# Kernel tuning notes

Hardware: AMD Instinct MI355X
Metric: run time of the kernel (lower is better)

## Reference

```python
import jax, jax.numpy as jnp
import numpy as np
from jax import lax

B, T, V, E, H, O = 32, 64, 30000, 64, 64, 7


def setup_inputs() -> dict:
    key = jax.random.key(0)
    ks = jax.random.split(key, 17)
    s_in = 1.0 / np.sqrt(E)
    s_h = 1.0 / np.sqrt(H)
    inp = {
        "x": jax.random.uniform(ks[0], (B, T, V), dtype=jnp.float32),
        "vocab_embed": 0.02 * jax.random.normal(ks[1], (V, E), dtype=jnp.float32),
        "W_ir": s_in * jax.random.normal(ks[2], (H, E), dtype=jnp.float32),
        "W_iz": s_in * jax.random.normal(ks[3], (H, E), dtype=jnp.float32),
        "W_in": s_in * jax.random.normal(ks[4], (H, E), dtype=jnp.float32),
        "W_hr": s_h * jax.random.normal(ks[5], (H, H), dtype=jnp.float32),
        "W_hz": s_h * jax.random.normal(ks[6], (H, H), dtype=jnp.float32),
        "W_hn": s_h * jax.random.normal(ks[7], (H, H), dtype=jnp.float32),
        "b_ir": s_h * jax.random.normal(ks[8], (H,), dtype=jnp.float32),
        "b_iz": s_h * jax.random.normal(ks[9], (H,), dtype=jnp.float32),
        "b_in": s_h * jax.random.normal(ks[10], (H,), dtype=jnp.float32),
        "b_hr": s_h * jax.random.normal(ks[11], (H,), dtype=jnp.float32),
        "b_hz": s_h * jax.random.normal(ks[12], (H,), dtype=jnp.float32),
        "b_hn": s_h * jax.random.normal(ks[13], (H,), dtype=jnp.float32),
        "W_out": s_h * jax.random.normal(ks[14], (O, H), dtype=jnp.float32),
        "b_out": s_h * jax.random.normal(ks[15], (O,), dtype=jnp.float32),
        "prediction_point": T,
    }
    return inp


def reference(x, vocab_embed, W_ir, W_iz, W_in, W_hr, W_hz, W_hn,
              b_ir, b_iz, b_in, b_hr, b_hz, b_hn, W_out, b_out,
              prediction_point):
    # embed_x = relu((x @ vocab_embed) / x.sum(-1, keepdims))  -> [B, T, E]
    embed_x = jax.nn.relu(jnp.einsum("btv,ve->bte", x, vocab_embed)
                          / jnp.sum(x, axis=2, keepdims=True))

    # t = 0: no hidden contribution at all (faithful to original)
    e0 = embed_x[:, 0, :]
    z1 = jax.nn.sigmoid(e0 @ W_iz.T + b_iz)
    n1 = jnp.tanh(e0 @ W_in.T + b_in)
    h0 = (1.0 - z1) * n1  # [B, H]

    def step(h, e_t):
        hr = h @ W_hr.T + b_hr
        r = jax.nn.sigmoid(e_t @ W_ir.T + b_ir + hr)
        z = jax.nn.sigmoid(e_t @ W_iz.T + b_iz + h @ W_hz.T + b_hz)
        # NOTE: original code uses hidden_reset (W_hr) here, not hidden_new
        n = jnp.tanh(e_t @ W_in.T + b_in + r * hr)
        h_new = (1.0 - z) * n + z * h
        return h_new, None

    # scan over t = 1 .. prediction_point-1
    es = jnp.swapaxes(embed_x[:, 1:prediction_point, :], 0, 1)  # [T-1, B, E]
    h_final, _ = lax.scan(step, h0, es)

    return h_final @ W_out.T + b_out  # [B, O] logits (prob=False)
```

## Files before the change

### kernel.cpp

```cpp
#include <hip/hip_runtime.h>
#include <hip/hip_bf16.h>

typedef unsigned short u16;
typedef short short8 __attribute__((ext_vector_type(8)));
typedef float floatx4 __attribute__((ext_vector_type(4)));

#define BB 32
#define TT 64
#define VV 30000
#define EE 64
#define HH 64
#define OO 7
#define KSPLIT 32
#define NU32 937
#define KTAIL0 29984

__device__ __forceinline__ u16 f2b(float f) {
    unsigned u = __float_as_uint(f);
    u += 0x7FFFu + ((u >> 16) & 1u);
    return (u16)(u >> 16);
}

__device__ __forceinline__ float sigmoid_f(float x) {
    return 1.f / (1.f + __expf(-x));
}

__device__ __forceinline__ float tanh_f(float x) {
    float a = fabsf(x);
    float e = __expf(-2.f * a);
    float t = (1.f - e) / (1.f + e);
    return x < 0.f ? -t : t;
}

__global__ __launch_bounds__(256) void kT(const float* __restrict__ VE, u16* __restrict__ VT) {
    __shared__ u16 tile[64][72];
    int v0 = blockIdx.x * 64;
    int t = threadIdx.x;
    #pragma unroll
    for (int i = 0; i < 4; ++i) {
        int c = i * 256 + t;
        int row = c >> 4, col4 = (c & 15) * 4;
        if (v0 + row < VV) {
            float4 d = *(const float4*)(VE + (size_t)(v0 + row) * EE + col4);
            ushort4 s;
            s.x = f2b(d.x); s.y = f2b(d.y); s.z = f2b(d.z); s.w = f2b(d.w);
            *(ushort4*)&tile[row][col4] = s;
        }
    }
    __syncthreads();
    int e0 = (t >> 6) * 16;
    int v = t & 63;
    if (v0 + v < VV) {
        #pragma unroll
        for (int ee = 0; ee < 16; ++ee) {
            int e = e0 + ee;
            VT[(size_t)e * VV + v0 + v] = tile[v][e];
        }
    }
}

__global__ __launch_bounds__(256) void kE(const float* __restrict__ x, const u16* __restrict__ vt,
                                          float* __restrict__ Cpart, float* __restrict__ Rpart) {
    int tid = threadIdx.x;
    int w = tid >> 6, l = tid & 63;
    int r15 = l & 15, q = l >> 4;
    int mb = blockIdx.x, kb = blockIdx.y;
    int m0 = mb * 64;
    int wr = m0 + w * 16;

    const float* aRow = x + (size_t)(wr + r15) * VV;
    const u16* b0p = vt + (size_t)(r15)      * VV;
    const u16* b1p = vt + (size_t)(16 + r15) * VV;
    const u16* b2p = vt + (size_t)(32 + r15) * VV;
    const u16* b3p = vt + (size_t)(48 + r15) * VV;

    floatx4 acc[4] = {};
    floatx4 accS = {};
    short8 ones;
    #pragma unroll
    for (int i = 0; i < 8; ++i) ones[i] = (short)0x3F80;

    int u0 = (kb * NU32) / KSPLIT, u1 = ((kb + 1) * NU32) / KSPLIT;

    #pragma unroll 2
    for (int u = u0; u < u1; ++u) {
        int k0 = u * 32 + q * 8;
        float4 a0 = *(const float4*)(aRow + k0);
        float4 a1 = *(const float4*)(aRow + k0 + 4);
        short8 bf0 = *(const short8*)(b0p + k0);
        short8 bf1 = *(const short8*)(b1p + k0);
        short8 bf2 = *(const short8*)(b2p + k0);
        short8 bf3 = *(const short8*)(b3p + k0);
        short8 af;
        af[0] = (short)f2b(a0.x); af[1] = (short)f2b(a0.y);
        af[2] = (short)f2b(a0.z); af[3] = (short)f2b(a0.w);
        af[4] = (short)f2b(a1.x); af[5] = (short)f2b(a1.y);
        af[6] = (short)f2b(a1.z); af[7] = (short)f2b(a1.w);
        acc[0] = __builtin_amdgcn_mfma_f32_16x16x32_bf16(af, bf0, acc[0], 0, 0, 0);
        acc[1] = __builtin_amdgcn_mfma_f32_16x16x32_bf16(af, bf1, acc[1], 0, 0, 0);
        acc[2] = __builtin_amdgcn_mfma_f32_16x16x32_bf16(af, bf2, acc[2], 0, 0, 0);
        acc[3] = __builtin_amdgcn_mfma_f32_16x16x32_bf16(af, bf3, acc[3], 0, 0, 0);
        accS   = __builtin_amdgcn_mfma_f32_16x16x32_bf16(af, ones, accS, 0, 0, 0);
    }

    if (kb == KSPLIT - 1) {
        short8 af, bf0, bf1, bf2, bf3;
        #pragma unroll
        for (int i = 0; i < 8; ++i) { af[i] = 0; bf0[i] = 0; bf1[i] = 0; bf2[i] = 0; bf3[i] = 0; }
        if (q < 2) {
            int k0 = KTAIL0 + q * 8;
            float4 a0 = *(const float4*)(aRow + k0);
            float4 a1 = *(const float4*)(aRow + k0 + 4);
            af[0] = (short)f2b(a0.x); af[1] = (short)f2b(a0.y);
            af[2] = (short)f2b(a0.z); af[3] = (short)f2b(a0.w);
            af[4] = (short)f2b(a1.x); af[5] = (short)f2b(a1.y);
            af[6] = (short)f2b(a1.z); af[7] = (short)f2b(a1.w);
            bf0 = *(const short8*)(b0p + k0);
            bf1 = *(const short8*)(b1p + k0);
            bf2 = *(const short8*)(b2p + k0);
            bf3 = *(const short8*)(b3p + k0);
        }
        acc[0] = __builtin_amdgcn_mfma_f32_16x16x32_bf16(af, bf0, acc[0], 0, 0, 0);
        acc[1] = __builtin_amdgcn_mfma_f32_16x16x32_bf16(af, bf1, acc[1], 0, 0, 0);
        acc[2] = __builtin_amdgcn_mfma_f32_16x16x32_bf16(af, bf2, acc[2], 0, 0, 0);
        acc[3] = __builtin_amdgcn_mfma_f32_16x16x32_bf16(af, bf3, acc[3], 0, 0, 0);
        accS   = __builtin_amdgcn_mfma_f32_16x16x32_bf16(af, ones, accS, 0, 0, 0);
    }

    float* Cp = Cpart + (size_t)kb * (2048 * 64);
    #pragma unroll
    for (int r = 0; r < 4; ++r) {
        int row = wr + q * 4 + r;
        #pragma unroll
        for (int n = 0; n < 4; ++n)
            Cp[(size_t)row * 64 + n * 16 + r15] = acc[n][r];
        if (r15 == 0) Rpart[kb * 2048 + row] = accS[r];
    }
}

__global__ __launch_bounds__(64) void kG(const float* __restrict__ Cpart, const float* __restrict__ Rpart,
                                         const float* __restrict__ Wir, const float* __restrict__ Wiz,
                                         const float* __restrict__ Win,
                                         const float* __restrict__ bir, const float* __restrict__ biz,
                                         const float* __restrict__ bin,
                                         float* __restrict__ Xr, float* __restrict__ Xz,
                                         float* __restrict__ Xn, float* __restrict__ H0) {
    int m = blockIdx.x;
    int j = threadIdx.x;
    __shared__ float e[64];
    float c = 0.f, rs = 0.f;
    #pragma unroll
    for (int kb = 0; kb < KSPLIT; ++kb) {
        c  += Cpart[(size_t)kb * 2048 * 64 + m * 64 + j];
        rs += Rpart[kb * 2048 + m];
    }
    float ev = c / rs;
    e[j] = ev > 0.f ? ev : 0.f;
    __syncthreads();
    float ar = bir[j], az = biz[j], an = bin[j];
    #pragma unroll 4
    for (int i = 0; i < 64; ++i) {
        float ei = e[i];
        ar += ei * Wir[j * 64 + i];
        az += ei * Wiz[j * 64 + i];
        an += ei * Win[j * 64 + i];
    }
    Xr[m * 64 + j] = ar;
    Xz[m * 64 + j] = az;
    Xn[m * 64 + j] = an;
    if ((m & 63) == 0) {
        int b = m >> 6;
        float z1 = sigmoid_f(az);
        float n1 = tanh_f(an);
        H0[b * 64 + j] = (1.f - z1) * n1;
    }
}

__global__ __launch_bounds__(256) void kS(const float* __restrict__ Xr, const float* __restrict__ Xz,
                                          const float* __restrict__ Xn, const float* __restrict__ H0,
                                          const float* __restrict__ Whr, const float* __restrict__ Whz,
                                          const float* __restrict__ bhr, const float* __restrict__ bhz,
                                          const float* __restrict__ Wout, const float* __restrict__ bout,
                                          float* __restrict__ out) {
    int b = blockIdx.x;
    int tid = threadIdx.x;
    int i = tid & 63, jw = tid >> 6;
    __shared__ float XsR[64 * 64], XsZ[64 * 64], XsN[64 * 64];
    __shared__ float h[64];
    __shared__ float P[4][2][64];

    const float* xr = Xr + (size_t)b * 4096;
    const float* xz = Xz + (size_t)b * 4096;
    const float* xn = Xn + (size_t)b * 4096;
    #pragma unroll
    for (int it = 0; it < 4; ++it) {
        int off = it * 1024 + tid * 4;
        *(float4*)&XsR[off] = *(const float4*)&xr[off];
        *(float4*)&XsZ[off] = *(const float4*)&xz[off];
        *(float4*)&XsN[off] = *(const float4*)&xn[off];
    }
    float wr[16], wz[16];
    #pragma unroll
    for (int jj = 0; jj < 16; ++jj) {
        wr[jj] = Whr[i * 64 + jw * 16 + jj];
        wz[jj] = Whz[i * 64 + jw * 16 + jj];
    }
    float bhr_i = bhr[i];
    float bhz_i = bhz[i];
    if (tid < 64) h[tid] = H0[b * 64 + tid];
    __syncthreads();

    for (int t = 1; t < 64; ++t) {
        float pr = 0.f, pz = 0.f;
        #pragma unroll
        for (int jj = 0; jj < 16; ++jj) {
            float hj = h[jw * 16 + jj];
            pr += hj * wr[jj];
            pz += hj * wz[jj];
        }
        P[jw][0][i] = pr;
        P[jw][1][i] = pz;
        __syncthreads();
        if (tid < 64) {
            float hr = bhr_i + P[0][0][i] + P[1][0][i] + P[2][0][i] + P[3][0][i];
            float hz = bhz_i + P[0][1][i] + P[1][1][i] + P[2][1][i] + P[3][1][i];
            float r = sigmoid_f(XsR[t * 64 + i] + hr);
            float z = sigmoid_f(XsZ[t * 64 + i] + hz);
            float n = tanh_f(XsN[t * 64 + i] + r * hr);
            h[i] = (1.f - z) * n + z * h[i];
        }
        __syncthreads();
    }

    if (tid < OO) {
        float acc2 = bout[tid];
        #pragma unroll 8
        for (int ii = 0; ii < 64; ++ii)
            acc2 += h[ii] * Wout[tid * 64 + ii];
        out[b * OO + tid] = acc2;
    }
}

extern "C" void kernel_launch(void* const* d_in, const int* in_sizes, int n_in,
                              void* d_out, int out_size, void* d_ws, size_t ws_size,
                              hipStream_t stream) {
    const float* x    = (const float*)d_in[0];
    const float* VE   = (const float*)d_in[1];
    const float* Wir  = (const float*)d_in[2];
    const float* Wiz  = (const float*)d_in[3];
    const float* Win  = (const float*)d_in[4];
    const float* Whr  = (const float*)d_in[5];
    const float* Whz  = (const float*)d_in[6];
    const float* bir  = (const float*)d_in[8];
    const float* biz  = (const float*)d_in[9];
    const float* bin  = (const float*)d_in[10];
    const float* bhr  = (const float*)d_in[11];
    const float* bhz  = (const float*)d_in[12];
    const float* Wout = (const float*)d_in[14];
    const float* bout = (const float*)d_in[15];

    char* ws = (char*)d_ws;
    u16*   VT    = (u16*)(ws);
    float* Cpart = (float*)(ws + 3840000);
    float* Rpart = (float*)(ws + 3840000 + 16777216);
    float* Xr    = (float*)(ws + 20879360);
    float* Xz    = (float*)(ws + 21403648);
    float* Xn    = (float*)(ws + 21927936);
    float* H0    = (float*)(ws + 22452224);

    kT<<<(VV + 63) / 64, 256, 0, stream>>>(VE, VT);
    kE<<<dim3(2048 / 64, KSPLIT), 256, 0, stream>>>(x, VT, Cpart, Rpart);
    kG<<<2048, 64, 0, stream>>>(Cpart, Rpart, Wir, Wiz, Win, bir, biz, bin, Xr, Xz, Xn, H0);
    kS<<<BB, 256, 0, stream>>>(Xr, Xz, Xn, H0, Whr, Whz, bhr, bhz, Wout, bout, (float*)d_out);
}
```

Before: 450.2 us.

## Pack bf16 with byte-permute truncation and rewrite gate projection with MFMA

In the main embedding GEMM, the per-element round-to-nearest fp32→bf16 conversion is replaced by a single byte-permute that packs the high halves of two floats. This cuts VALU work in the inner loop but switches to truncation, which adds a small rounding bias. The input-gate projection kernel is rewritten to handle 64 rows per block. It reduces the split-K partials with float4 loads, stages normalized, ReLU'd embeddings in LDS as bf16, and computes all three gate projections with MFMA instead of scalar FMA loops. This lowers instruction count and launch granularity, but it runs only 32 blocks to stream the 16 MB partial buffer and uses bf16 weights in place of fp32.

```diff
diff --git a/kernel.cpp b/kernel.cpp
--- a/kernel.cpp
+++ b/kernel.cpp
@@ -19,6 +19,10 @@
     unsigned u = __float_as_uint(f);
     u += 0x7FFFu + ((u >> 16) & 1u);
     return (u16)(u >> 16);
+}
+
+__device__ __forceinline__ unsigned pk2(float fo, float fe) {
+    return __builtin_amdgcn_perm(__float_as_uint(fo), __float_as_uint(fe), 0x07060302u);
 }
 
 __device__ __forceinline__ float sigmoid_f(float x) {
@@ -92,10 +96,11 @@
         short8 bf2 = *(const short8*)(b2p + k0);
         short8 bf3 = *(const short8*)(b3p + k0);
         short8 af;
-        af[0] = (short)f2b(a0.x); af[1] = (short)f2b(a0.y);
-        af[2] = (short)f2b(a0.z); af[3] = (short)f2b(a0.w);
-        af[4] = (short)f2b(a1.x); af[5] = (short)f2b(a1.y);
-        af[6] = (short)f2b(a1.z); af[7] = (short)f2b(a1.w);
+        unsigned* afu = (unsigned*)&af;
+        afu[0] = pk2(a0.y, a0.x);
+        afu[1] = pk2(a0.w, a0.z);
+        afu[2] = pk2(a1.y, a1.x);
+        afu[3] = pk2(a1.w, a1.z);
         acc[0] = __builtin_amdgcn_mfma_f32_16x16x32_bf16(af, bf0, acc[0], 0, 0, 0);
         acc[1] = __builtin_amdgcn_mfma_f32_16x16x32_bf16(af, bf1, acc[1], 0, 0, 0);
         acc[2] = __builtin_amdgcn_mfma_f32_16x16x32_bf16(af, bf2, acc[2], 0, 0, 0);
@@ -111,10 +116,11 @@
             int k0 = KTAIL0 + q * 8;
             float4 a0 = *(const float4*)(aRow + k0);
             float4 a1 = *(const float4*)(aRow + k0 + 4);
-            af[0] = (short)f2b(a0.x); af[1] = (short)f2b(a0.y);
-            af[2] = (short)f2b(a0.z); af[3] = (short)f2b(a0.w);
-            af[4] = (short)f2b(a1.x); af[5] = (short)f2b(a1.y);
-            af[6] = (short)f2b(a1.z); af[7] = (short)f2b(a1.w);
+            unsigned* afu = (unsigned*)&af;
+            afu[0] = pk2(a0.y, a0.x);
+            afu[1] = pk2(a0.w, a0.z);
+            afu[2] = pk2(a1.y, a1.x);
+            afu[3] = pk2(a1.w, a1.z);
             bf0 = *(const short8*)(b0p + k0);
             bf1 = *(const short8*)(b1p + k0);
             bf2 = *(const short8*)(b2p + k0);
@@ -138,41 +144,102 @@
     }
 }
 
-__global__ __launch_bounds__(64) void kG(const float* __restrict__ Cpart, const float* __restrict__ Rpart,
-                                         const float* __restrict__ Wir, const float* __restrict__ Wiz,
-                                         const float* __restrict__ Win,
-                                         const float* __restrict__ bir, const float* __restrict__ biz,
-                                         const float* __restrict__ bin,
-                                         float* __restrict__ Xr, float* __restrict__ Xz,
-                                         float* __restrict__ Xn, float* __restrict__ H0) {
-    int m = blockIdx.x;
-    int j = threadIdx.x;
-    __shared__ float e[64];
-    float c = 0.f, rs = 0.f;
-    #pragma unroll
+__global__ __launch_bounds__(256) void kG2(const float* __restrict__ Cpart, const float* __restrict__ Rpart,
+                                           const float* __restrict__ Wir, const float* __restrict__ Wiz,
+                                           const float* __restrict__ Win,
+                                           const float* __restrict__ bir, const float* __restrict__ biz,
+                                           const float* __restrict__ bin,
+                                           float* __restrict__ Xr, float* __restrict__ Xz,
+                                           float* __restrict__ Xn, float* __restrict__ H0) {
+    __shared__ __align__(16) u16 eL[64 * 72];
+    __shared__ float rsinv[64];
+    int tid = threadIdx.x;
+    int m0 = blockIdx.x * 64;
+
+    if (tid < 64) {
+        float rs = 0.f;
+        #pragma unroll
+        for (int kb = 0; kb < KSPLIT; ++kb)
+            rs += Rpart[kb * 2048 + m0 + tid];
+        rsinv[tid] = 1.f / rs;
+    }
+    float4 a4[4];
+    #pragma unroll
+    for (int r = 0; r < 4; ++r) { a4[r].x = 0.f; a4[r].y = 0.f; a4[r].z = 0.f; a4[r].w = 0.f; }
+    const float* cp = Cpart + (size_t)m0 * 64 + tid * 4;
+    #pragma unroll 4
     for (int kb = 0; kb < KSPLIT; ++kb) {
-        c  += Cpart[(size_t)kb * 2048 * 64 + m * 64 + j];
-        rs += Rpart[kb * 2048 + m];
-    }
-    float ev = c / rs;
-    e[j] = ev > 0.f ? ev : 0.f;
+        #pragma unroll
+        for (int r = 0; r < 4; ++r) {
+            float4 v = *(const float4*)(cp + (size_t)kb * (2048 * 64) + r * 1024);
+            a4[r].x += v.x; a4[r].y += v.y; a4[r].z += v.z; a4[r].w += v.w;
+        }
+    }
     __syncthreads();
-    float ar = bir[j], az = biz[j], an = bin[j];
-    #pragma unroll 4
-    for (int i = 0; i < 64; ++i) {
-        float ei = e[i];
-        ar += ei * Wir[j * 64 + i];
-        az += ei * Wiz[j * 64 + i];
-        an += ei * Win[j * 64 + i];
-    }
-    Xr[m * 64 + j] = ar;
-    Xz[m * 64 + j] = az;
-    Xn[m * 64 + j] = an;
-    if ((m & 63) == 0) {
-        int b = m >> 6;
-        float z1 = sigmoid_f(az);
-        float n1 = tanh_f(an);
-        H0[b * 64 + j] = (1.f - z1) * n1;
+    #pragma unroll
+    for (int r = 0; r < 4; ++r) {
+        int m = r * 16 + (tid >> 4);
+        float ri = rsinv[m];
+        float e0 = a4[r].x * ri, e1 = a4[r].y * ri, e2 = a4[r].z * ri, e3 = a4[r].w * ri;
+        e0 = e0 > 0.f ? e0 : 0.f;  e1 = e1 > 0.f ? e1 : 0.f;
+        e2 = e2 > 0.f ? e2 : 0.f;  e3 = e3 > 0.f ? e3 : 0.f;
+        ushort4 s;
+        s.x = f2b(e0); s.y = f2b(e1); s.z = f2b(e2); s.w = f2b(e3);
+        *(ushort4*)&eL[m * 72 + (tid & 15) * 4] = s;
+    }
+    __syncthreads();
+
+    int w = tid >> 6, l = tid & 63;
+    int r15 = l & 15, q = l >> 4;
+    short8 a0 = *(const short8*)&eL[(w * 16 + r15) * 72 + q * 8];
+    short8 a1 = *(const short8*)&eL[(w * 16 + r15) * 72 + 32 + q * 8];
+
+    floatx4 acc[3][4] = {};
+    const float* Wg0 = Wir; const float* Wg1 = Wiz; const float* Wg2 = Win;
+    #pragma unroll
+    for (int g = 0; g < 3; ++g) {
+        const float* W = (g == 0) ? Wg0 : (g == 1) ? Wg1 : Wg2;
+        #pragma unroll
+        for (int nb = 0; nb < 4; ++nb) {
+            const float* wrow = W + (nb * 16 + r15) * 64 + q * 8;
+            float4 w0 = *(const float4*)(wrow);
+            float4 w1 = *(const float4*)(wrow + 4);
+            float4 w2 = *(const float4*)(wrow + 32);
+            float4 w3 = *(const float4*)(wrow + 36);
+            short8 b0, b1;
+            unsigned* b0u = (unsigned*)&b0; unsigned* b1u = (unsigned*)&b1;
+            b0u[0] = pk2(w0.y, w0.x); b0u[1] = pk2(w0.w, w0.z);
+            b0u[2] = pk2(w1.y, w1.x); b0u[3] = pk2(w1.w, w1.z);
+            b1u[0] = pk2(w2.y, w2.x); b1u[1] = pk2(w2.w, w2.z);
+            b1u[2] = pk2(w3.y, w3.x); b1u[3] = pk2(w3.w, w3.z);
+            acc[g][nb] = __builtin_amdgcn_mfma_f32_16x16x32_bf16(a0, b0, acc[g][nb], 0, 0, 0);
+            acc[g][nb] = __builtin_amdgcn_mfma_f32_16x16x32_bf16(a1, b1, acc[g][nb], 0, 0, 0);
+        }
+    }
+
+    #pragma unroll
+    for (int g = 0; g < 3; ++g) {
+        float* Xo = (g == 0) ? Xr : (g == 1) ? Xz : Xn;
+        const float* bo = (g == 0) ? bir : (g == 1) ? biz : bin;
+        #pragma unroll
+        for (int nb = 0; nb < 4; ++nb) {
+            int j = nb * 16 + r15;
+            float bias = bo[j];
+            #pragma unroll
+            for (int r = 0; r < 4; ++r) {
+                int m = m0 + w * 16 + q * 4 + r;
+                Xo[(size_t)m * 64 + j] = acc[g][nb][r] + bias;
+            }
+        }
+    }
+    if (w == 0 && q == 0) {
+        #pragma unroll
+        for (int nb = 0; nb < 4; ++nb) {
+            int j = nb * 16 + r15;
+            float z1 = sigmoid_f(acc[1][nb][0] + biz[j]);
+            float n1 = tanh_f(acc[2][nb][0] + bin[j]);
+            H0[blockIdx.x * 64 + j] = (1.f - z1) * n1;
+        }
     }
 }
 
@@ -270,6 +337,6 @@
 
     kT<<<(VV + 63) / 64, 256, 0, stream>>>(VE, VT);
     kE<<<dim3(2048 / 64, KSPLIT), 256, 0, stream>>>(x, VT, Cpart, Rpart);
-    kG<<<2048, 64, 0, stream>>>(Cpart, Rpart, Wir, Wiz, Win, bir, biz, bin, Xr, Xz, Xn, H0);
+    kG2<<<32, 256, 0, stream>>>(Cpart, Rpart, Wir, Wiz, Win, bir, biz, bin, Xr, Xz, Xn, H0);
     kS<<<BB, 256, 0, stream>>>(Xr, Xz, Xn, H0, Whr, Whz, bhr, bhz, Wout, bout, (float*)d_out);
 }
```

Measured after the change: 447.4 us. Within noise of the previous version (-0.6%).
